# Performance work log

Hardware: AMD Instinct MI355X
Metric: run time of the kernel (lower is better)

Reference implementation:

```python
import jax, jax.numpy as jnp
import numpy as np

N_NODES = 100_000
N_EDGES = 1_600_000
N_RELS = 16
D_IN = 128
D_OUT = 64


def setup_inputs() -> dict:
    key = jax.random.key(0)
    k_feat, k_w, k_src, k_dst, k_et = jax.random.split(key, 5)
    feat = jax.random.normal(k_feat, (N_NODES, D_IN), dtype=jnp.float32)
    weight = jax.random.normal(k_w, (N_RELS, D_IN, D_OUT), dtype=jnp.float32)
    src = jax.random.randint(k_src, (N_EDGES,), 0, N_NODES, dtype=jnp.int32)
    dst = jax.random.randint(k_dst, (N_EDGES,), 0, N_NODES, dtype=jnp.int32)
    etypes = jnp.sort(jax.random.randint(k_et, (N_EDGES,), 0, N_RELS, dtype=jnp.int32))
    return {"feat": feat, "weight": weight, "src": src, "dst": dst, "etypes": etypes}


def reference(feat, weight, src, dst, etypes):
    # RGCN gather-mm: message m_e = feat[src_e] @ W[etype_e]; out_v = sum_{e: dst_e = v} m_e
    # Efficient form: project all nodes with all relation weights (dense GEMM, small R),
    # then gather the (etype, src) slice per edge and segment-sum into destinations.
    proj = jnp.einsum('nd,rde->rne', feat, weight)          # [R, N, d_out]
    msg = proj[etypes, src]                                  # [E, d_out] irregular gather
    out = jax.ops.segment_sum(msg, dst, num_segments=feat.shape[0])  # [N, d_out] scatter-sum
    return out
```

## Files before the change

### kernel.cpp

```cpp
#include <hip/hip_runtime.h>
#include <hip/hip_bf16.h>


#define NTHREADS 256
#define TM 64

typedef __attribute__((ext_vector_type(8))) __bf16 bf16x8;
typedef __attribute__((ext_vector_type(4))) float f32x4;

__global__ void cvt_w_kernel(const float* __restrict__ w,
                             __bf16* __restrict__ o, int total) {
    int idx = blockIdx.x * 256 + threadIdx.x;
    if (idx >= total) return;
    int r = idx >> 13;
    int rem = idx & 8191;
    int k = rem >> 6;
    int n = rem & 63;
    o[(r << 13) + (n << 7) + k] = (__bf16)w[idx];
}

__global__ __launch_bounds__(NTHREADS)
void proj_all_kernel(const float* __restrict__ feat, const __bf16* __restrict__ wtb,
                     const unsigned char* __restrict__ usedb,
                     int N, int R, __bf16* __restrict__ projb) {
    __shared__ __bf16 Wt[2][64 * 136];
    __shared__ unsigned used_l[16 * 32];

    int t = threadIdx.x;
    int wave = t >> 6, lane = t & 63;
    int q = lane >> 4, m = lane & 15;
    long blk0 = (long)blockIdx.x * 128;
    long node0 = blk0 + wave * 32;

    for (int c = t; c < R * 32; c += NTHREADS) {
        int rr = c >> 5, i = c & 31;
        used_l[rr * 32 + i] = *(const unsigned*)(usedb + (size_t)rr * N + blk0 + i * 4);
    }

    bf16x8 a[2][4];
    #pragma unroll
    for (int mt = 0; mt < 2; mt++) {
        long nd = node0 + mt * 16 + m;
        if (nd > N - 1) nd = N - 1;
        const float* arow = feat + nd * 128;
        #pragma unroll
        for (int ks = 0; ks < 4; ks++) {
            float4 fa = *(const float4*)(arow + ks * 32 + q * 8);
            float4 fb = *(const float4*)(arow + ks * 32 + q * 8 + 4);
            bf16x8 v;
            v[0] = (__bf16)fa.x; v[1] = (__bf16)fa.y; v[2] = (__bf16)fa.z; v[3] = (__bf16)fa.w;
            v[4] = (__bf16)fb.x; v[5] = (__bf16)fb.y; v[6] = (__bf16)fb.z; v[7] = (__bf16)fb.w;
            a[mt][ks] = v;
        }
    }

    {
        const __bf16* wg = wtb;
        #pragma unroll
        for (int i = 0; i < 4; i++) {
            int c = t + i * 256;
            int n = c >> 4, kc = c & 15;
            *(bf16x8*)(&Wt[0][n * 136 + kc * 8]) = *(const bf16x8*)(wg + n * 128 + kc * 8);
        }
    }
    asm volatile("s_waitcnt lgkmcnt(0)" ::: "memory");
    __builtin_amdgcn_s_barrier();
    __builtin_amdgcn_sched_barrier(0);

    for (int r = 0; r < R; r++) {
        int cur = r & 1, nxt = cur ^ 1;
        bool pf = (r + 1 < R);

        bf16x8 wreg[4];
        if (pf) {
            const __bf16* wg = wtb + ((size_t)(r + 1) << 13);
            #pragma unroll
            for (int i = 0; i < 4; i++) {
                int c = t + i * 256;
                int n = c >> 4, kc = c & 15;
                wreg[i] = *(const bf16x8*)(wg + n * 128 + kc * 8);
            }
        }

        f32x4 acc[2][4] = {};
        #pragma unroll
        for (int ks = 0; ks < 4; ks++) {
            bf16x8 b0 = *(const bf16x8*)(&Wt[cur][(0 * 16 + m) * 136 + ks * 32 + q * 8]);
            bf16x8 b1 = *(const bf16x8*)(&Wt[cur][(1 * 16 + m) * 136 + ks * 32 + q * 8]);
            bf16x8 b2 = *(const bf16x8*)(&Wt[cur][(2 * 16 + m) * 136 + ks * 32 + q * 8]);
            bf16x8 b3 = *(const bf16x8*)(&Wt[cur][(3 * 16 + m) * 136 + ks * 32 + q * 8]);
            #pragma unroll
            for (int mt = 0; mt < 2; mt++) {
                acc[mt][0] = __builtin_amdgcn_mfma_f32_16x16x32_bf16(a[mt][ks], b0, acc[mt][0], 0, 0, 0);
                acc[mt][1] = __builtin_amdgcn_mfma_f32_16x16x32_bf16(a[mt][ks], b1, acc[mt][1], 0, 0, 0);
                acc[mt][2] = __builtin_amdgcn_mfma_f32_16x16x32_bf16(a[mt][ks], b2, acc[mt][2], 0, 0, 0);
                acc[mt][3] = __builtin_amdgcn_mfma_f32_16x16x32_bf16(a[mt][ks], b3, acc[mt][3], 0, 0, 0);
            }
        }

        #pragma unroll
        for (int mt = 0; mt < 2; mt++) {
            unsigned g = used_l[r * 32 + ((wave * 32 + mt * 16 + q * 4) >> 2)];
            #pragma unroll
            for (int reg = 0; reg < 4; reg++) {
                long nd = node0 + mt * 16 + q * 4 + reg;
                if (nd < N && ((g >> (reg * 8)) & 1)) {
                    union { unsigned long long u; __bf16 h[4]; } pk;
                    pk.h[0] = (__bf16)acc[mt][0][reg];
                    pk.h[1] = (__bf16)acc[mt][1][reg];
                    pk.h[2] = (__bf16)acc[mt][2][reg];
                    pk.h[3] = (__bf16)acc[mt][3][reg];
                    *(unsigned long long*)(projb + ((size_t)r * N + nd) * 64 + m * 4) = pk.u;
                }
            }
        }

        if (pf) {
            #pragma unroll
            for (int i = 0; i < 4; i++) {
                int c = t + i * 256;
                int n = c >> 4, kc = c & 15;
                *(bf16x8*)(&Wt[nxt][n * 136 + kc * 8]) = wreg[i];
            }
            asm volatile("s_waitcnt lgkmcnt(0)" ::: "memory");
            __builtin_amdgcn_s_barrier();
            __builtin_amdgcn_sched_barrier(0);
        }
    }
}

__global__ __launch_bounds__(1024)
void bucket_hist(const int* __restrict__ dst, int E, int* __restrict__ bhist) {
    __shared__ int lh[1024];
    int t = threadIdx.x;
    lh[t] = 0;
    __syncthreads();
    long base = (long)blockIdx.x * 8192;
    #pragma unroll
    for (int i = 0; i < 8; i++) {
        long e = base + t + 1024 * i;
        if (e < E) atomicAdd(&lh[dst[e] >> 7], 1);
    }
    __syncthreads();
    if (lh[t]) atomicAdd(&bhist[t], lh[t]);
}

__global__ __launch_bounds__(1024)
void bucket_scan(const int* __restrict__ bhist, int NB, int N, int E,
                 int* __restrict__ boff, int* __restrict__ bcur,
                 int* __restrict__ dofs) {
    __shared__ int sm[1024];
    int t = threadIdx.x;
    int v = (t < NB) ? bhist[t] : 0;
    sm[t] = v;
    __syncthreads();
    for (int s = 1; s < 1024; s <<= 1) {
        int add = (t >= s) ? sm[t - s] : 0;
        __syncthreads();
        sm[t] += add;
        __syncthreads();
    }
    if (t < NB) { int ex = sm[t] - v; boff[t] = ex; bcur[t] = ex; }
    if (t == 0) { boff[NB] = E; dofs[N] = E; }
}

__global__ __launch_bounds__(1024)
void bucket_scatter(const int* __restrict__ dst, const int* __restrict__ src,
                    const int* __restrict__ etypes, int E, int N, int NB,
                    int* __restrict__ bcur, int* __restrict__ items,
                    unsigned char* __restrict__ usedb) {
    __shared__ int lh[1024], lb[1024];
    int t = threadIdx.x;
    lh[t] = 0;
    __syncthreads();
    long base = (long)blockIdx.x * 8192;
    int bs[8], it[8];
    #pragma unroll
    for (int i = 0; i < 8; i++) {
        long e = base + t + 1024 * i;
        if (e < E) {
            int d = dst[e];
            int bkt = d >> 7;
            bs[i] = bkt;
            int pair = etypes[e] * N + src[e];
            it[i] = ((d & 127) << 24) | pair;
            usedb[pair] = 1;
            atomicAdd(&lh[bkt], 1);
        } else bs[i] = -1;
    }
    __syncthreads();
    for (int bb = t; bb < NB; bb += 1024) {
        int c = lh[bb];
        lb[bb] = c ? atomicAdd(&bcur[bb], c) : 0;
        lh[bb] = 0;
    }
    __syncthreads();
    #pragma unroll
    for (int i = 0; i < 8; i++) {
        if (bs[i] >= 0) {
            int pos = lb[bs[i]] + atomicAdd(&lh[bs[i]], 1);
            items[pos] = it[i];
        }
    }
}

__global__ __launch_bounds__(256)
void refine_kernel(const int* __restrict__ boff, const int* __restrict__ items,
                   int N, int* __restrict__ pidx, int* __restrict__ dofs) {
    __shared__ int h[128], sc[128], cur[128];
    int b = blockIdx.x, t = threadIdx.x;
    int j0 = boff[b], j1 = boff[b + 1];
    if (t < 128) h[t] = 0;
    __syncthreads();
    for (int j = j0 + t; j < j1; j += 256)
        atomicAdd(&h[((unsigned)items[j]) >> 24], 1);
    __syncthreads();
    if (t < 128) sc[t] = h[t];
    __syncthreads();
    for (int s = 1; s < 128; s <<= 1) {
        int add = (t >= s && t < 128) ? sc[t - s] : 0;
        __syncthreads();
        if (t < 128) sc[t] += add;
        __syncthreads();
    }
    if (t < 128) {
        int ex = sc[t] - h[t];
        cur[t] = ex;
        int v = (b << 7) + t;
        if (v < N) dofs[v] = j0 + ex;
    }
    __syncthreads();
    for (int j = j0 + t; j < j1; j += 256) {
        int it = items[j];
        int dl = ((unsigned)it) >> 24;
        int pos = j0 + atomicAdd(&cur[dl], 1);
        pidx[pos] = it & 0xFFFFFF;
    }
}

__global__ __launch_bounds__(256)
void reduce_kernel(const int* __restrict__ dofs, const int* __restrict__ pidx,
                   const __bf16* __restrict__ projb, int N, float* __restrict__ out) {
    int gid = blockIdx.x * 256 + threadIdx.x;
    int sg = gid >> 3, c8 = gid & 7;
    int nsg = (gridDim.x * 256) >> 3;
    for (int v = sg; v < N; v += nsg) {
        int j0 = dofs[v], j1 = dofs[v + 1];
        float acc[8] = {0.f, 0.f, 0.f, 0.f, 0.f, 0.f, 0.f, 0.f};
        int j = j0;
        for (; j + 1 < j1; j += 2) {
            int p0 = pidx[j], p1 = pidx[j + 1];
            bf16x8 v0 = *(const bf16x8*)(projb + (size_t)p0 * 64 + c8 * 8);
            bf16x8 v1 = *(const bf16x8*)(projb + (size_t)p1 * 64 + c8 * 8);
            #pragma unroll
            for (int i = 0; i < 8; i++) acc[i] += (float)v0[i] + (float)v1[i];
        }
        if (j < j1) {
            int p = pidx[j];
            bf16x8 v0 = *(const bf16x8*)(projb + (size_t)p * 64 + c8 * 8);
            #pragma unroll
            for (int i = 0; i < 8; i++) acc[i] += (float)v0[i];
        }
        float* orow = out + (size_t)v * 64;
        #pragma unroll
        for (int i = 0; i < 8; i++) {
            int cp = c8 * 8 + i;
            orow[(cp & 3) * 16 + (cp >> 2)] = acc[i];
        }
    }
}

__global__ __launch_bounds__(NTHREADS)
void rgcn_atomic(const float* __restrict__ feat, const float* __restrict__ weight,
                 const int* __restrict__ src, const int* __restrict__ dst,
                 const int* __restrict__ etypes, int E,
                 float* __restrict__ out) {
    __shared__ __bf16 Wt[64 * 136];
    int b = blockIdx.x;
    int e0 = b * TM;
    int t = threadIdx.x;
    int wave = t >> 6, lane = t & 63;
    int q = lane >> 4, m = lane & 15;
    int wbase = e0 + wave * 16;
    int last = e0 + TM - 1; if (last > E - 1) last = E - 1;
    int rmin = etypes[e0];
    int rmax = etypes[last];
    int em = wbase + m;
    bool rowok = em < E;
    int ei = rowok ? em : E - 1;
    int my_et = rowok ? etypes[em] : -1;
    const float* arow = feat + (long)src[ei] * 128;
    bf16x8 a[4];
    #pragma unroll
    for (int ks = 0; ks < 4; ks++) {
        float4 fa = *(const float4*)(arow + ks * 32 + q * 8);
        float4 fb = *(const float4*)(arow + ks * 32 + q * 8 + 4);
        bf16x8 v;
        v[0] = (__bf16)fa.x; v[1] = (__bf16)fa.y;
        v[2] = (__bf16)fa.z; v[3] = (__bf16)fa.w;
        v[4] = (__bf16)fb.x; v[5] = (__bf16)fb.y;
        v[6] = (__bf16)fb.z; v[7] = (__bf16)fb.w;
        a[ks] = v;
    }
    f32x4 acc0 = {0.f, 0.f, 0.f, 0.f};
    f32x4 acc1 = {0.f, 0.f, 0.f, 0.f};
    f32x4 acc2 = {0.f, 0.f, 0.f, 0.f};
    f32x4 acc3 = {0.f, 0.f, 0.f, 0.f};
    for (int r = rmin; r <= rmax; ++r) {
        if (r != rmin) __syncthreads();
        const float* wg = weight + (r << 13);
        for (int p = t; p < 4096; p += NTHREADS) {
            int n = p & 63, kh = p >> 6;
            float w0 = wg[(kh * 2) * 64 + n];
            float w1 = wg[(kh * 2 + 1) * 64 + n];
            union { unsigned u; __bf16 h[2]; } pk;
            pk.h[0] = (__bf16)w0; pk.h[1] = (__bf16)w1;
            *(unsigned*)&Wt[n * 136 + kh * 2] = pk.u;
        }
        __syncthreads();
        bool on = (my_et == r);
        #pragma unroll
        for (int ks = 0; ks < 4; ks++) {
            bf16x8 af = a[ks];
            if (!on) {
                #pragma unroll
                for (int j = 0; j < 8; j++) af[j] = (__bf16)0.f;
            }
            bf16x8 b0 = *(const bf16x8*)(&Wt[(0 * 16 + m) * 136 + ks * 32 + q * 8]);
            bf16x8 b1 = *(const bf16x8*)(&Wt[(1 * 16 + m) * 136 + ks * 32 + q * 8]);
            bf16x8 b2 = *(const bf16x8*)(&Wt[(2 * 16 + m) * 136 + ks * 32 + q * 8]);
            bf16x8 b3 = *(const bf16x8*)(&Wt[(3 * 16 + m) * 136 + ks * 32 + q * 8]);
            acc0 = __builtin_amdgcn_mfma_f32_16x16x32_bf16(af, b0, acc0, 0, 0, 0);
            acc1 = __builtin_amdgcn_mfma_f32_16x16x32_bf16(af, b1, acc1, 0, 0, 0);
            acc2 = __builtin_amdgcn_mfma_f32_16x16x32_bf16(af, b2, acc2, 0, 0, 0);
            acc3 = __builtin_amdgcn_mfma_f32_16x16x32_bf16(af, b3, acc3, 0, 0, 0);
        }
    }
    #pragma unroll
    for (int reg = 0; reg < 4; reg++) {
        int er = wbase + q * 4 + reg;
        if (er < E) {
            float* orow = out + (long)dst[er] * 64;
            unsafeAtomicAdd(orow + 0 * 16 + m, acc0[reg]);
            unsafeAtomicAdd(orow + 1 * 16 + m, acc1[reg]);
            unsafeAtomicAdd(orow + 2 * 16 + m, acc2[reg]);
            unsafeAtomicAdd(orow + 3 * 16 + m, acc3[reg]);
        }
    }
}

extern "C" void kernel_launch(void* const* d_in, const int* in_sizes, int n_in,
                              void* d_out, int out_size, void* d_ws, size_t ws_size,
                              hipStream_t stream) {
    const float* feat   = (const float*)d_in[0];
    const float* weight = (const float*)d_in[1];
    const int*   src    = (const int*)d_in[2];
    const int*   dst    = (const int*)d_in[3];
    const int*   etypes = (const int*)d_in[4];
    float* out = (float*)d_out;

    int nfeat = in_sizes[0];
    int nw    = in_sizes[1];
    int E     = in_sizes[2];
    int N     = nfeat / 128;
    int R     = nw >> 13;
    int NB    = (N + 127) >> 7;

    size_t o = 0;
    auto take = [&](size_t bytes) { size_t r = o; o = (o + bytes + 255) & ~(size_t)255; return r; };
    size_t o_bhist = take((size_t)NB * 4);
    size_t o_usedb = take((size_t)R * N);
    size_t o_boff  = take((size_t)(NB + 1) * 4);
    size_t o_bcur  = take((size_t)NB * 4);
    size_t o_dofs  = take((size_t)(N + 1) * 4);
    size_t o_items = take((size_t)E * 4);
    size_t o_pidx  = take((size_t)E * 4);
    size_t o_wtb   = take((size_t)nw * 2);
    size_t o_projb = take((size_t)R * N * 64 * 2);
    size_t need = o;

    bool fast = (ws_size >= need) && (NB <= 1024) && ((size_t)R * N < (1u << 24)) && (R <= 16);

    if (fast) {
        char* ws = (char*)d_ws;
        int* bhist = (int*)(ws + o_bhist);
        unsigned char* usedb = (unsigned char*)(ws + o_usedb);
        int* boff  = (int*)(ws + o_boff);
        int* bcur  = (int*)(ws + o_bcur);
        int* dofs  = (int*)(ws + o_dofs);
        int* items = (int*)(ws + o_items);
        int* pidx  = (int*)(ws + o_pidx);
        __bf16* wtb   = (__bf16*)(ws + o_wtb);
        __bf16* projb = (__bf16*)(ws + o_projb);

        int cgrid = (int)(((long)E + 8191) / 8192);

        hipMemsetAsync(bhist, 0, (size_t)NB * 4, stream);
        hipMemsetAsync(usedb, 0, (size_t)R * N, stream);
        bucket_hist<<<cgrid, 1024, 0, stream>>>(dst, E, bhist);
        bucket_scan<<<1, 1024, 0, stream>>>(bhist, NB, N, E, boff, bcur, dofs);
        bucket_scatter<<<cgrid, 1024, 0, stream>>>(dst, src, etypes, E, N, NB, bcur, items, usedb);
        refine_kernel<<<NB, 256, 0, stream>>>(boff, items, N, pidx, dofs);
        cvt_w_kernel<<<(nw + 255) / 256, 256, 0, stream>>>(weight, wtb, nw);

        proj_all_kernel<<<(N + 127) / 128, NTHREADS, 0, stream>>>(feat, wtb, usedb, N, R, projb);
        int rblk = (N + 31) / 32;
        reduce_kernel<<<rblk, 256, 0, stream>>>(dofs, pidx, projb, N, out);
    } else {
        hipMemsetAsync(d_out, 0, (size_t)out_size * sizeof(float), stream);
        int mgrid = (E + TM - 1) / TM;
        rgcn_atomic<<<mgrid, NTHREADS, 0, stream>>>(feat, weight, src, dst, etypes, E, out);
    }
}
```

Before: 252.6 us.

## Fuse per-bucket refine sort into reduce kernel using shared-memory chunks

Drops the separate refine kernel, which wrote a destination-sorted pidx array plus dofs offsets to global memory. A new bucket_reduce kernel now counting-sorts each 128-destination bucket's items into shared memory in chunks of CH items and gathers/sums the projected rows straight from there. This saves a kernel launch and a global write/read pass over E indices. In exchange, the reduce grid shrinks to NB blocks (about 782) of 512 threads with a 2-node-per-thread layout, and extra syncs and per-chunk scans may reduce parallelism for the gather.

Result: no change. 253.4 us (+0.3%).

```diff
diff --git a/kernel.cpp b/kernel.cpp
--- a/kernel.cpp
+++ b/kernel.cpp
@@ -4,6 +4,7 @@
 
 #define NTHREADS 256
 #define TM 64
+#define CH 2560
 
 typedef __attribute__((ext_vector_type(8))) __bf16 bf16x8;
 typedef __attribute__((ext_vector_type(4))) float f32x4;
@@ -146,9 +147,8 @@
 }
 
 __global__ __launch_bounds__(1024)
-void bucket_scan(const int* __restrict__ bhist, int NB, int N, int E,
-                 int* __restrict__ boff, int* __restrict__ bcur,
-                 int* __restrict__ dofs) {
+void bucket_scan(const int* __restrict__ bhist, int NB, int E,
+                 int* __restrict__ boff, int* __restrict__ bcur) {
     __shared__ int sm[1024];
     int t = threadIdx.x;
     int v = (t < NB) ? bhist[t] : 0;
@@ -161,7 +161,7 @@
         __syncthreads();
     }
     if (t < NB) { int ex = sm[t] - v; boff[t] = ex; bcur[t] = ex; }
-    if (t == 0) { boff[NB] = E; dofs[N] = E; }
+    if (t == 0) { boff[NB] = E; }
 }
 
 __global__ __launch_bounds__(1024)
@@ -204,68 +204,90 @@
     }
 }
 
-__global__ __launch_bounds__(256)
-void refine_kernel(const int* __restrict__ boff, const int* __restrict__ items,
-                   int N, int* __restrict__ pidx, int* __restrict__ dofs) {
+__global__ __launch_bounds__(512)
+void bucket_reduce(const int* __restrict__ boff, const int* __restrict__ items,
+                   const __bf16* __restrict__ projb, int N,
+                   float* __restrict__ out) {
     __shared__ int h[128], sc[128], cur[128];
+    __shared__ int its[CH];
     int b = blockIdx.x, t = threadIdx.x;
     int j0 = boff[b], j1 = boff[b + 1];
-    if (t < 128) h[t] = 0;
-    __syncthreads();
-    for (int j = j0 + t; j < j1; j += 256)
-        atomicAdd(&h[((unsigned)items[j]) >> 24], 1);
-    __syncthreads();
-    if (t < 128) sc[t] = h[t];
-    __syncthreads();
-    for (int s = 1; s < 128; s <<= 1) {
-        int add = (t >= s && t < 128) ? sc[t - s] : 0;
-        __syncthreads();
-        if (t < 128) sc[t] += add;
-        __syncthreads();
-    }
-    if (t < 128) {
-        int ex = sc[t] - h[t];
-        cur[t] = ex;
-        int v = (b << 7) + t;
-        if (v < N) dofs[v] = j0 + ex;
-    }
-    __syncthreads();
-    for (int j = j0 + t; j < j1; j += 256) {
-        int it = items[j];
-        int dl = ((unsigned)it) >> 24;
-        int pos = j0 + atomicAdd(&cur[dl], 1);
-        pidx[pos] = it & 0xFFFFFF;
-    }
-}
-
-__global__ __launch_bounds__(256)
-void reduce_kernel(const int* __restrict__ dofs, const int* __restrict__ pidx,
-                   const __bf16* __restrict__ projb, int N, float* __restrict__ out) {
-    int gid = blockIdx.x * 256 + threadIdx.x;
-    int sg = gid >> 3, c8 = gid & 7;
-    int nsg = (gridDim.x * 256) >> 3;
-    for (int v = sg; v < N; v += nsg) {
-        int j0 = dofs[v], j1 = dofs[v + 1];
-        float acc[8] = {0.f, 0.f, 0.f, 0.f, 0.f, 0.f, 0.f, 0.f};
-        int j = j0;
-        for (; j + 1 < j1; j += 2) {
-            int p0 = pidx[j], p1 = pidx[j + 1];
-            bf16x8 v0 = *(const bf16x8*)(projb + (size_t)p0 * 64 + c8 * 8);
-            bf16x8 v1 = *(const bf16x8*)(projb + (size_t)p1 * 64 + c8 * 8);
+    int sub = t >> 3, c8 = t & 7;
+
+    float acc[2][8] = {};
+
+    for (int c0 = j0; c0 < j1; c0 += CH) {
+        int n = j1 - c0; if (n > CH) n = CH;
+
+        if (t < 128) h[t] = 0;
+        __syncthreads();
+
+        int my[CH / 512];
+        int dl[CH / 512];
+        #pragma unroll
+        for (int i = 0; i < CH / 512; i++) {
+            int k = t + i * 512;
+            if (k < n) {
+                my[i] = items[c0 + k];
+                dl[i] = ((unsigned)my[i]) >> 24;
+                atomicAdd(&h[dl[i]], 1);
+            } else dl[i] = -1;
+        }
+        __syncthreads();
+
+        if (t < 128) sc[t] = h[t];
+        __syncthreads();
+        for (int s = 1; s < 128; s <<= 1) {
+            int add = (t >= s && t < 128) ? sc[t - s] : 0;
+            __syncthreads();
+            if (t < 128) sc[t] += add;
+            __syncthreads();
+        }
+        if (t < 128) cur[t] = sc[t] - h[t];
+        __syncthreads();
+
+        #pragma unroll
+        for (int i = 0; i < CH / 512; i++) {
+            if (dl[i] >= 0) {
+                int pos = atomicAdd(&cur[dl[i]], 1);
+                its[pos] = my[i] & 0xFFFFFF;
+            }
+        }
+        __syncthreads();
+
+        #pragma unroll
+        for (int idx = 0; idx < 2; idx++) {
+            int d = sub + idx * 64;
+            int s = sc[d] - h[d];
+            int e = sc[d];
+            int k = s;
+            for (; k + 1 < e; k += 2) {
+                int p0 = its[k], p1 = its[k + 1];
+                bf16x8 v0 = *(const bf16x8*)(projb + (size_t)p0 * 64 + c8 * 8);
+                bf16x8 v1 = *(const bf16x8*)(projb + (size_t)p1 * 64 + c8 * 8);
+                #pragma unroll
+                for (int i = 0; i < 8; i++) acc[idx][i] += (float)v0[i] + (float)v1[i];
+            }
+            if (k < e) {
+                int p = its[k];
+                bf16x8 v0 = *(const bf16x8*)(projb + (size_t)p * 64 + c8 * 8);
+                #pragma unroll
+                for (int i = 0; i < 8; i++) acc[idx][i] += (float)v0[i];
+            }
+        }
+        __syncthreads();
+    }
+
+    #pragma unroll
+    for (int idx = 0; idx < 2; idx++) {
+        long v = (long)b * 128 + sub + idx * 64;
+        if (v < N) {
+            float* orow = out + (size_t)v * 64;
             #pragma unroll
-            for (int i = 0; i < 8; i++) acc[i] += (float)v0[i] + (float)v1[i];
-        }
-        if (j < j1) {
-            int p = pidx[j];
-            bf16x8 v0 = *(const bf16x8*)(projb + (size_t)p * 64 + c8 * 8);
-            #pragma unroll
-            for (int i = 0; i < 8; i++) acc[i] += (float)v0[i];
-        }
-        float* orow = out + (size_t)v * 64;
-        #pragma unroll
-        for (int i = 0; i < 8; i++) {
-            int cp = c8 * 8 + i;
-            orow[(cp & 3) * 16 + (cp >> 2)] = acc[i];
+            for (int i = 0; i < 8; i++) {
+                int cp = c8 * 8 + i;
+                orow[(cp & 3) * 16 + (cp >> 2)] = acc[idx][i];
+            }
         }
     }
 }
@@ -372,9 +394,7 @@
     size_t o_usedb = take((size_t)R * N);
     size_t o_boff  = take((size_t)(NB + 1) * 4);
     size_t o_bcur  = take((size_t)NB * 4);
-    size_t o_dofs  = take((size_t)(N + 1) * 4);
     size_t o_items = take((size_t)E * 4);
-    size_t o_pidx  = take((size_t)E * 4);
     size_t o_wtb   = take((size_t)nw * 2);
     size_t o_projb = take((size_t)R * N * 64 * 2);
     size_t need = o;
@@ -387,9 +407,7 @@
         unsigned char* usedb = (unsigned char*)(ws + o_usedb);
         int* boff  = (int*)(ws + o_boff);
         int* bcur  = (int*)(ws + o_bcur);
-        int* dofs  = (int*)(ws + o_dofs);
         int* items = (int*)(ws + o_items);
-        int* pidx  = (int*)(ws + o_pidx);
         __bf16* wtb   = (__bf16*)(ws + o_wtb);
         __bf16* projb = (__bf16*)(ws + o_projb);
 
@@ -398,14 +416,12 @@
         hipMemsetAsync(bhist, 0, (size_t)NB * 4, stream);
         hipMemsetAsync(usedb, 0, (size_t)R * N, stream);
         bucket_hist<<<cgrid, 1024, 0, stream>>>(dst, E, bhist);
-        bucket_scan<<<1, 1024, 0, stream>>>(bhist, NB, N, E, boff, bcur, dofs);
+        bucket_scan<<<1, 1024, 0, stream>>>(bhist, NB, E, boff, bcur);
         bucket_scatter<<<cgrid, 1024, 0, stream>>>(dst, src, etypes, E, N, NB, bcur, items, usedb);
-        refine_kernel<<<NB, 256, 0, stream>>>(boff, items, N, pidx, dofs);
         cvt_w_kernel<<<(nw + 255) / 256, 256, 0, stream>>>(weight, wtb, nw);
 
         proj_all_kernel<<<(N + 127) / 128, NTHREADS, 0, stream>>>(feat, wtb, usedb, N, R, projb);
-        int rblk = (N + 31) / 32;
-        reduce_kernel<<<rblk, 256, 0, stream>>>(dofs, pidx, projb, N, out);
+        bucket_reduce<<<NB, 512, 0, stream>>>(boff, items, projb, N, out);
     } else {
         hipMemsetAsync(d_out, 0, (size_t)out_size * sizeof(float), stream);
         int mgrid = (E + TM - 1) / TM;
```
